# Optimization experiments

Hardware: AMD Instinct MI355X
Metric: run time of the kernel (lower is better)

## Reference

```python
import jax, jax.numpy as jnp
import numpy as np

D = 256; NHEAD = 8; NQ = 300; NLAYERS = 6; NLEV = 3; NPTS = 4
DFF = 1024; NCLS = 80; BS = 16
SPATIAL = ((80, 80), (40, 40), (20, 20))
LM = sum(h * w for h, w in SPATIAL)
DH = D // NHEAD
PARAM_NAMES = ['sa_wq','sa_bq','sa_wk','sa_bk','sa_wv','sa_bv','sa_wo','sa_bo',
               'ln1_g','ln1_b','ln2_g','ln2_b','ln3_g','ln3_b',
               'off_w','off_b','attw_w','attw_b','val_w','val_b','out_w','out_b',
               'ffn_w1','ffn_b1','ffn_w2','ffn_b2',
               'bb_w1','bb_b1','bb_w2','bb_b2','bb_w3','bb_b3',
               'sc_w','sc_b','qp_w1','qp_b1','qp_w2','qp_b2']


def _ln(x, g, b, eps=1e-5):
    m = x.mean(-1, keepdims=True)
    v = ((x - m) ** 2).mean(-1, keepdims=True)
    return (x - m) * jax.lax.rsqrt(v + eps) * g + b


def _mlp2(x, w1, b1, w2, b2):
    # 2-layer MLP, ReLU on hidden only (act_final_layer=False)
    return jnp.maximum(x @ w1 + b1, 0.0) @ w2 + b2


def _inv_sigmoid(x, eps=1e-5):
    x = jnp.clip(x, 0.0, 1.0)
    return jnp.log(jnp.clip(x, eps, None) / jnp.clip(1.0 - x, eps, None))


def _mha(q, k, v, wq, bq, wk, bk, wv, bv, wo, bo):
    B, N, _ = q.shape
    Q = (q @ wq + bq).reshape(B, N, NHEAD, DH)
    K = (k @ wk + bk).reshape(B, N, NHEAD, DH)
    V = (v @ wv + bv).reshape(B, N, NHEAD, DH)
    att = jnp.einsum('bqhd,bkhd->bhqk', Q, K) * (1.0 / np.sqrt(DH))
    att = jax.nn.softmax(att, axis=-1)
    o = jnp.einsum('bhqk,bkhd->bqhd', att, V).reshape(B, N, D)
    return o @ wo + bo


def _bilinear(v, x, y, Hl, Wl):
    # v: [B, Hl*Wl, C]; x, y: [B, M] pixel coords (align_corners=False, zero padding)
    x0 = jnp.floor(x); y0 = jnp.floor(y)
    wx = x - x0; wy = y - y0
    out = 0.0
    for dx, dy, w in ((0, 0, (1 - wx) * (1 - wy)), (1, 0, wx * (1 - wy)),
                      (0, 1, (1 - wx) * wy), (1, 1, wx * wy)):
        xi = x0 + dx; yi = y0 + dy
        valid = (xi >= 0) & (xi < Wl) & (yi >= 0) & (yi < Hl)
        lin = (jnp.clip(yi, 0, Hl - 1) * Wl + jnp.clip(xi, 0, Wl - 1)).astype(jnp.int32)
        g = jnp.take_along_axis(v, lin[..., None], axis=1)
        out = out + g * (w * valid)[..., None]
    return out


def _deform_attn(q, ref, memory, ow, ob, aw, ab, vw, vb, pw, pb):
    # q: [B,NQ,D]; ref: [B,NQ,4] cxcywh in [0,1]; memory: [B,LM,D]
    B = q.shape[0]
    value = (memory @ vw + vb).reshape(B, LM, NHEAD, DH)
    off = (q @ ow + ob).reshape(B, NQ, NHEAD, NLEV, NPTS, 2)
    attw = jax.nn.softmax((q @ aw + ab).reshape(B, NQ, NHEAD, NLEV * NPTS), -1)
    attw = attw.reshape(B, NQ, NHEAD, NLEV, NPTS)
    r = ref[:, :, None, None, None, :]
    loc = r[..., :2] + off / NPTS * r[..., 2:] * 0.5  # [B,NQ,H,LV,P,2]
    start = 0
    acc = 0.0
    for lv, (Hl, Wl) in enumerate(SPATIAL):
        v = value[:, start:start + Hl * Wl]  # [B, Hl*Wl, H, DH]
        v = v.transpose(0, 2, 1, 3).reshape(B * NHEAD, Hl * Wl, DH)
        g = loc[:, :, :, lv]  # [B,NQ,H,P,2]
        x = (g[..., 0] * Wl - 0.5).transpose(0, 2, 1, 3).reshape(B * NHEAD, NQ * NPTS)
        y = (g[..., 1] * Hl - 0.5).transpose(0, 2, 1, 3).reshape(B * NHEAD, NQ * NPTS)
        s = _bilinear(v, x, y, Hl, Wl).reshape(B, NHEAD, NQ, NPTS, DH)
        w = attw[:, :, :, lv].transpose(0, 2, 1, 3)  # [B,H,NQ,P]
        acc = acc + (s * w[..., None]).sum(3)  # [B,H,NQ,DH]
        start += Hl * Wl
    o = acc.transpose(0, 2, 1, 3).reshape(B, NQ, D)
    return o @ pw + pb


def _decoder(tgt, ref_points_unact, memory, p):
    ref_d = jax.nn.sigmoid(ref_points_unact)
    out = tgt
    for i in range(NLAYERS):
        pos = _mlp2(ref_d, p['qp_w1'], p['qp_b1'], p['qp_w2'], p['qp_b2'])
        q = out + pos
        t2 = _mha(q, q, out, p['sa_wq'][i], p['sa_bq'][i], p['sa_wk'][i], p['sa_bk'][i],
                  p['sa_wv'][i], p['sa_bv'][i], p['sa_wo'][i], p['sa_bo'][i])
        out = _ln(out + t2, p['ln1_g'][i], p['ln1_b'][i])
        t2 = _deform_attn(out + pos, ref_d, memory, p['off_w'][i], p['off_b'][i],
                          p['attw_w'][i], p['attw_b'][i], p['val_w'][i], p['val_b'][i],
                          p['out_w'][i], p['out_b'][i])
        out = _ln(out + t2, p['ln2_g'][i], p['ln2_b'][i])
        out = _ln(out + _mlp2(out, p['ffn_w1'][i], p['ffn_b1'][i], p['ffn_w2'][i], p['ffn_b2'][i]),
                  p['ln3_g'][i], p['ln3_b'][i])
        h = jnp.maximum(out @ p['bb_w1'][i] + p['bb_b1'][i], 0.0)
        h = jnp.maximum(h @ p['bb_w2'][i] + p['bb_b2'][i], 0.0)
        delta = h @ p['bb_w3'][i] + p['bb_b3'][i]
        ref_d = jax.nn.sigmoid(delta + _inv_sigmoid(ref_d))
    logits = out @ p['sc_w'][NLAYERS - 1] + p['sc_b'][NLAYERS - 1]
    return ref_d, logits


def setup_inputs():
    key = jax.random.key(0)
    keys = iter(jax.random.split(key, 64))
    def rn(shape, s=0.02):
        return jax.random.normal(next(keys), shape, jnp.float32) * s
    L = NLAYERS
    inp = {
        'tgt': rn((BS, NQ, D), 1.0),
        'ref_points_unact': rn((BS, NQ, 4), 1.0),
        'memory': rn((BS, LM, D), 1.0),
    }
    for n in ['sa_wq', 'sa_wk', 'sa_wv', 'sa_wo', 'val_w', 'out_w', 'bb_w1', 'bb_w2']:
        inp[n] = rn((L, D, D))
    for n in ['sa_bq', 'sa_bk', 'sa_bv', 'sa_bo', 'ln1_b', 'ln2_b', 'ln3_b',
              'val_b', 'out_b', 'ffn_b2', 'bb_b1', 'bb_b2']:
        inp[n] = jnp.zeros((L, D), jnp.float32)
    for n in ['ln1_g', 'ln2_g', 'ln3_g']:
        inp[n] = jnp.ones((L, D), jnp.float32)
    OFF = NHEAD * NLEV * NPTS * 2
    ATT = NHEAD * NLEV * NPTS
    inp['off_w'] = rn((L, D, OFF)); inp['off_b'] = rn((L, OFF), 0.1)
    inp['attw_w'] = rn((L, D, ATT)); inp['attw_b'] = jnp.zeros((L, ATT), jnp.float32)
    inp['ffn_w1'] = rn((L, D, DFF)); inp['ffn_b1'] = jnp.zeros((L, DFF), jnp.float32)
    inp['ffn_w2'] = rn((L, DFF, D))
    inp['bb_w3'] = rn((L, D, 4)); inp['bb_b3'] = jnp.zeros((L, 4), jnp.float32)
    inp['sc_w'] = rn((L, D, NCLS)); inp['sc_b'] = jnp.zeros((L, NCLS), jnp.float32)
    inp['qp_w1'] = rn((4, 2 * D)); inp['qp_b1'] = jnp.zeros((2 * D,), jnp.float32)
    inp['qp_w2'] = rn((2 * D, D)); inp['qp_b2'] = jnp.zeros((D,), jnp.float32)
    return inp


def reference(tgt, ref_points_unact, memory, sa_wq, sa_bq, sa_wk, sa_bk, sa_wv, sa_bv,
              sa_wo, sa_bo, ln1_g, ln1_b, ln2_g, ln2_b, ln3_g, ln3_b, off_w, off_b,
              attw_w, attw_b, val_w, val_b, out_w, out_b, ffn_w1, ffn_b1, ffn_w2, ffn_b2,
              bb_w1, bb_b1, bb_w2, bb_b2, bb_w3, bb_b3, sc_w, sc_b,
              qp_w1, qp_b1, qp_w2, qp_b2):
    _a = dict(locals())
    p = {k: _a[k] for k in PARAM_NAMES}
    ref_d, logits = _decoder(tgt, ref_points_unact, memory, p)
    # eval path: stacked final-layer outputs, shape [1, BS, NQ, 4] and [1, BS, NQ, NCLS]
    return ref_d[None], logits[None]
```

## Files before the change

### kernel.cpp

```cpp
#include <hip/hip_runtime.h>
#include <hip/hip_bf16.h>

typedef __hip_bfloat16 bf16;
typedef short short8 __attribute__((ext_vector_type(8)));
typedef short short4v __attribute__((ext_vector_type(4)));
typedef float float4v __attribute__((ext_vector_type(4)));

#define D_ 256
#define NHEAD_ 8
#define DH_ 32
#define NQ_ 300
#define NLAYERS_ 6
#define DFF_ 1024
#define NCLS_ 80
#define BS_ 16
#define LM_ 8400
#define BN_ (BS_*NQ_)

static __device__ __forceinline__ short f2bf(float x){
    union{float f; unsigned u;} v; v.f = x;
    unsigned r = v.u + 0x7FFF + ((v.u>>16)&1);
    return (short)(r>>16);
}
static __device__ __forceinline__ float bf2f(short s){
    union{unsigned u; float f;} v; v.u = ((unsigned)(unsigned short)s)<<16; return v.f;
}

#define LSTR 40

template<int TM, bool ABF16, bool RELU, bool OUTBF16>
__global__ __launch_bounds__(256) void mfma_gemm_kernel(
    const void* __restrict__ Av, const void* __restrict__ A2v,
    const void* __restrict__ A3v, int nA2lim,
    const short* __restrict__ WT, size_t zWT,
    const float* __restrict__ b0, const float* __restrict__ b1,
    const float* __restrict__ b2, int ns1, int ns2, size_t zB,
    void* __restrict__ Cv, size_t zC, int M, int K, int N, int nxt)
{
    __shared__ short As[2][TM*LSTR];
    __shared__ short Bs[2][128*LSTR];
    int zz, n0;
    if(nxt){ zz = blockIdx.x / nxt; n0 = (blockIdx.x % nxt)*128; }
    else   { zz = blockIdx.z;       n0 = blockIdx.x*128; }
    WT += (size_t)zz*zWT; b0 += (size_t)zz*zB; b1 += (size_t)zz*zB; b2 += (size_t)zz*zB;
    int tid = threadIdx.x;
    int lane = tid&63, wave = tid>>6;
    int m0 = blockIdx.y*TM;
    const int MI = TM/32;
    int wm = (wave>>1)*(TM/2), wn = (wave&1)*64;
    int lr = lane&15, lq = lane>>4;
    float4v acc[MI][4];
    #pragma unroll
    for(int i=0;i<MI;i++)
        #pragma unroll
        for(int j=0;j<4;j++){ acc[i][j].x=0.f; acc[i][j].y=0.f; acc[i][j].z=0.f; acc[i][j].w=0.f; }

    const float* Af; const float* Ad; const short* Ah;
    if(ABF16){ Ah = (const short*)Av; Af=nullptr; Ad=nullptr; }
    else {
        Af = (n0 < nA2lim)? (const float*)Av : (const float*)A3v;
        Ad = (n0 < nA2lim)? (const float*)A2v : nullptr;
        Ah = nullptr;
    }

    short8  rA16[ABF16? TM/64 : 1];
    float4v rAf [ABF16? 1 : TM/32];
    float4v rAd [ABF16? 1 : TM/32];
    short8  rB[2];

    auto LOAD = [&](int k0){
        if constexpr(ABF16){
            #pragma unroll
            for(int it=0; it<TM/64; ++it){
                int idx=(it*256+tid)*8; int r=idx>>5, kk=idx&31; int gm=m0+r;
                short8 v = {};
                if(gm<M) v = *(const short8*)(Ah + (size_t)gm*K + (k0+kk));
                rA16[it]=v;
            }
        } else {
            #pragma unroll
            for(int it=0; it<TM/32; ++it){
                int idx=(it*256+tid)*4; int r=idx>>5, kk=idx&31; int gm=m0+r;
                float4v v; v.x=0.f;v.y=0.f;v.z=0.f;v.w=0.f;
                float4v w; w.x=0.f;w.y=0.f;w.z=0.f;w.w=0.f;
                if(gm<M){
                    v = *(const float4v*)(Af + (size_t)gm*K + (k0+kk));
                    if(Ad) w = *(const float4v*)(Ad + (size_t)gm*K + (k0+kk));
                }
                rAf[it]=v; rAd[it]=w;
            }
        }
        #pragma unroll
        for(int it=0; it<2; ++it){
            int idx=(it*256+tid)*8; int r=idx>>5, kk=idx&31; int gn=n0+r;
            short8 v = {};
            if(gn<N) v = *(const short8*)(WT + (size_t)gn*K + (k0+kk));
            rB[it]=v;
        }
    };
    auto STORE = [&](int buf){
        if constexpr(ABF16){
            #pragma unroll
            for(int it=0; it<TM/64; ++it){
                int idx=(it*256+tid)*8; int r=idx>>5, kk=idx&31;
                *(short8*)(&As[buf][r*LSTR+kk]) = rA16[it];
            }
        } else {
            #pragma unroll
            for(int it=0; it<TM/32; ++it){
                int idx=(it*256+tid)*4; int r=idx>>5, kk=idx&31;
                float4v v = rAf[it];
                if(Ad){ v.x+=rAd[it].x; v.y+=rAd[it].y; v.z+=rAd[it].z; v.w+=rAd[it].w; }
                short4v h; h.x=f2bf(v.x); h.y=f2bf(v.y); h.z=f2bf(v.z); h.w=f2bf(v.w);
                *(short4v*)(&As[buf][r*LSTR+kk]) = h;
            }
        }
        #pragma unroll
        for(int it=0; it<2; ++it){
            int idx=(it*256+tid)*8; int r=idx>>5, kk=idx&31;
            *(short8*)(&Bs[buf][r*LSTR+kk]) = rB[it];
        }
    };

    const int nt = K>>5;
    LOAD(0);
    STORE(0);
    __syncthreads();
    for(int t=0; t<nt; ++t){
        int cb = t&1;
        if(t+1<nt) LOAD((t+1)<<5);
        short8 af[MI], bfr[4];
        #pragma unroll
        for(int mi=0;mi<MI;mi++) af[mi]  = *(const short8*)(&As[cb][(wm+mi*16+lr)*LSTR + lq*8]);
        #pragma unroll
        for(int ni=0;ni<4;ni++) bfr[ni] = *(const short8*)(&Bs[cb][(wn+ni*16+lr)*LSTR + lq*8]);
        #pragma unroll
        for(int mi=0;mi<MI;mi++)
            #pragma unroll
            for(int ni=0;ni<4;ni++)
                acc[mi][ni] = __builtin_amdgcn_mfma_f32_16x16x32_bf16(af[mi], bfr[ni], acc[mi][ni], 0,0,0);
        if(t+1<nt){
            STORE(cb^1);
            __syncthreads();
        }
    }
    float* Cf=(float*)Cv + (size_t)zz*zC; bf16* Ch=(bf16*)Cv + (size_t)zz*zC;
    #pragma unroll
    for(int mi=0;mi<MI;mi++){
        #pragma unroll
        for(int r=0;r<4;r++){
            int gm = m0+wm+mi*16+lq*4+r;
            if(gm>=M) continue;
            #pragma unroll
            for(int ni=0;ni<4;ni++){
                int gn = n0+wn+ni*16+lr;
                if(gn>=N) continue;
                float bv = (gn<ns1)? b0[gn] : ((gn<ns2)? b1[gn-ns1] : b2[gn-ns2]);
                float v = acc[mi][ni][r] + bv;
                if(RELU) v = fmaxf(v,0.f);
                if(OUTBF16) Ch[(size_t)gm*N+gn]=__float2bfloat16(v);
                else        Cf[(size_t)gm*N+gn]=v;
            }
        }
    }
}

__global__ __launch_bounds__(256) void fused_mha_kernel(
    const float* __restrict__ QKV, short* __restrict__ O)
{
    const int ld = 768;
    int bh = blockIdx.y; int b = bh>>3, h = bh&7;
    int q0 = blockIdx.x*64;
    __shared__ short lds[31104];
    short* Vts = lds;
    short* Qs  = lds + 10368;
    short* Ks  = lds + 12672;
    short* Ps  = lds + 10368;
    int tid = threadIdx.x;
    for(int idx=tid; idx<64*8; idx+=256){
        int r=idx>>3, c4=(idx&7)*4; int gq=q0+r;
        float4v v; v.x=0.f;v.y=0.f;v.z=0.f;v.w=0.f;
        if(gq<NQ_) v = *(const float4v*)(QKV + ((size_t)(b*NQ_+gq))*ld + h*DH_ + c4);
        short4v h4; h4.x=f2bf(v.x);h4.y=f2bf(v.y);h4.z=f2bf(v.z);h4.w=f2bf(v.w);
        *(short4v*)(Qs + r*36 + c4) = h4;
    }
    for(int idx=tid; idx<304*8; idx+=256){
        int r=idx>>3, c4=(idx&7)*4;
        float4v v; v.x=0.f;v.y=0.f;v.z=0.f;v.w=0.f;
        if(r<NQ_) v = *(const float4v*)(QKV + 256 + ((size_t)(b*NQ_+r))*ld + h*DH_ + c4);
        short4v h4; h4.x=f2bf(v.x);h4.y=f2bf(v.y);h4.z=f2bf(v.z);h4.w=f2bf(v.w);
        *(short4v*)(Ks + r*36 + c4) = h4;
    }
    for(int idx=tid; idx<320*8; idx+=256){
        int r=idx>>3, c4=(idx&7)*4;
        float4v v; v.x=0.f;v.y=0.f;v.z=0.f;v.w=0.f;
        if(r<NQ_) v = *(const float4v*)(QKV + 512 + ((size_t)(b*NQ_+r))*ld + h*DH_ + c4);
        Vts[(c4+0)*324+r]=f2bf(v.x); Vts[(c4+1)*324+r]=f2bf(v.y);
        Vts[(c4+2)*324+r]=f2bf(v.z); Vts[(c4+3)*324+r]=f2bf(v.w);
    }
    __syncthreads();

    int lane = tid&63, wave = tid>>6;
    int lr = lane&15, lq = lane>>4;
    int mrow = wave*16;
    const float scale = 0.17677669529663687f;

    float4v acc[19];
    #pragma unroll
    for(int t=0;t<19;t++){ acc[t].x=0.f; acc[t].y=0.f; acc[t].z=0.f; acc[t].w=0.f; }
    short8 afrag = *(const short8*)(&Qs[(mrow+lr)*36 + lq*8]);
    #pragma unroll
    for(int t=0;t<19;t++){
        short8 bfrag = *(const short8*)(&Ks[(t*16+lr)*36 + lq*8]);
        acc[t] = __builtin_amdgcn_mfma_f32_16x16x32_bf16(afrag, bfrag, acc[t], 0,0,0);
    }
    __syncthreads();

    for(int idx=tid; idx<64*16; idx+=256){
        int r=idx>>4, c=idx&15;
        Ps[r*324 + 304 + c]=0;
    }
    #pragma unroll
    for(int t=0;t<19;t++){
        #pragma unroll
        for(int r=0;r<4;r++) acc[t][r] *= scale;
    }
    if(lr>=12){
        #pragma unroll
        for(int r=0;r<4;r++) acc[18][r] = -1e30f;
    }
    float mx[4];
    #pragma unroll
    for(int r=0;r<4;r++){
        float m = acc[0][r];
        #pragma unroll
        for(int t=1;t<19;t++) m = fmaxf(m, acc[t][r]);
        m = fmaxf(m, __shfl_xor(m,1)); m = fmaxf(m, __shfl_xor(m,2));
        m = fmaxf(m, __shfl_xor(m,4)); m = fmaxf(m, __shfl_xor(m,8));
        mx[r]=m;
    }
    float sum[4] = {0.f,0.f,0.f,0.f};
    #pragma unroll
    for(int t=0;t<19;t++){
        #pragma unroll
        for(int r=0;r<4;r++){
            float p = __expf(acc[t][r]-mx[r]);
            acc[t][r]=p; sum[r]+=p;
        }
    }
    #pragma unroll
    for(int r=0;r<4;r++){
        float s = sum[r];
        s += __shfl_xor(s,1); s += __shfl_xor(s,2);
        s += __shfl_xor(s,4); s += __shfl_xor(s,8);
        sum[r] = 1.f/s;
    }
    #pragma unroll
    for(int t=0;t<19;t++){
        #pragma unroll
        for(int r=0;r<4;r++){
            Ps[(mrow + lq*4 + r)*324 + t*16 + lr] = f2bf(acc[t][r]*sum[r]);
        }
    }
    __syncthreads();
    float4v oacc[2];
    oacc[0].x=0.f;oacc[0].y=0.f;oacc[0].z=0.f;oacc[0].w=0.f;
    oacc[1]=oacc[0];
    #pragma unroll
    for(int kc=0;kc<10;kc++){
        short8 pa = *(const short8*)(&Ps[(mrow+lr)*324 + kc*32 + lq*8]);
        #pragma unroll
        for(int n=0;n<2;n++){
            short8 vb = *(const short8*)(&Vts[(n*16+lr)*324 + kc*32 + lq*8]);
            oacc[n] = __builtin_amdgcn_mfma_f32_16x16x32_bf16(pa, vb, oacc[n], 0,0,0);
        }
    }
    #pragma unroll
    for(int n=0;n<2;n++){
        #pragma unroll
        for(int r=0;r<4;r++){
            int gq = q0 + mrow + lq*4 + r;
            if(gq<NQ_)
                O[((size_t)(b*NQ_+gq))*D_ + h*DH_ + n*16 + lr] = f2bf(oacc[n][r]);
        }
    }
}

#define NTD 74
struct TD { const float* src; unsigned dstoff; int K, N, base; };
struct TAll { TD d[NTD]; };

__global__ __launch_bounds__(256) void transpose_all_kernel(TAll p, short* __restrict__ WTb){
    int blk = blockIdx.x;
    int di = 0;
    #pragma unroll 1
    for(int i=0;i<NTD;i++){ if(blk >= p.d[i].base) di = i; }
    TD d = p.d[di];
    int rel = blk - d.base;
    int ntx = (d.N+31)/32;
    int tn = (rel % ntx)*32, tk = (rel / ntx)*32;
    __shared__ float t[32][33];
    int tx = threadIdx.x&31, ty = threadIdx.x>>5;
    for(int i=0;i<32;i+=8){
        int k = tk+ty+i, n = tn+tx;
        t[ty+i][tx] = (k<d.K && n<d.N)? d.src[(size_t)k*d.N+n] : 0.f;
    }
    __syncthreads();
    short* out = WTb + d.dstoff;
    for(int i=0;i<32;i+=8){
        int n = tn+ty+i, k = tk+tx;
        if(n<d.N && k<d.K) out[(size_t)n*d.K+k] = f2bf(t[tx][ty+i]);
    }
}

template<bool RELU, bool BBOX>
__global__ __launch_bounds__(256) void gemm_kernel(
    const float* __restrict__ A, const float* __restrict__ W,
    const float* __restrict__ bias, float* __restrict__ Cf,
    int M, int K, int N)
{
    __shared__ float As[16][68];
    __shared__ float Bs[16][68];
    int tid = threadIdx.x;
    int m0 = blockIdx.y*64, n0 = blockIdx.x*64;
    int tm = tid>>4, tn = tid&15;
    float acc[4][4] = {};
    int lam = tid>>2;
    int lak = (tid&3)*4;
    int lbk = tid>>4;
    int lbn = (tid&15)*4;
    for(int k0=0;k0<K;k0+=16){
        {
            int m = m0+lam;
            #pragma unroll
            for(int j=0;j<4;j++){
                int k = k0+lak+j;
                float v=0.f;
                if(m<M && k<K) v = A[(size_t)m*K+k];
                As[lak+j][lam]=v;
            }
        }
        {
            int k = k0+lbk;
            #pragma unroll
            for(int j=0;j<4;j++){
                int n = n0+lbn+j;
                float v=0.f;
                if(k<K && n<N) v = W[(size_t)k*N+n];
                Bs[lbk][lbn+j]=v;
            }
        }
        __syncthreads();
        #pragma unroll
        for(int kk=0;kk<16;kk++){
            float a[4], bb[4];
            #pragma unroll
            for(int i=0;i<4;i++) a[i]=As[kk][tm*4+i];
            #pragma unroll
            for(int j=0;j<4;j++) bb[j]=Bs[kk][tn*4+j];
            #pragma unroll
            for(int i=0;i<4;i++)
                #pragma unroll
                for(int j=0;j<4;j++) acc[i][j] += a[i]*bb[j];
        }
        __syncthreads();
    }
    #pragma unroll
    for(int i=0;i<4;i++){
        int m=m0+tm*4+i; if(m>=M) continue;
        #pragma unroll
        for(int j=0;j<4;j++){
            int n=n0+tn*4+j; if(n>=N) continue;
            float v = acc[i][j] + bias[n];
            if(BBOX){
                float x = Cf[(size_t)m*N+n];
                x = fminf(fmaxf(x,0.f),1.f);
                float num = fmaxf(x,1e-5f), den = fmaxf(1.f-x,1e-5f);
                float nd = v + logf(num/den);
                Cf[(size_t)m*N+n] = 1.f/(1.f+expf(-nd));
            } else {
                if(RELU) v = fmaxf(v,0.f);
                Cf[(size_t)m*N+n]=v;
            }
        }
    }
}

__global__ void copy_kernel(const float* __restrict__ a, float* __restrict__ o, int n){
    int i = blockIdx.x*blockDim.x+threadIdx.x;
    if(i<n) o[i]=a[i];
}
__global__ void cvt_f32_bf16_kernel(const float* __restrict__ a, short* __restrict__ o, int n4){
    int i = blockIdx.x*blockDim.x+threadIdx.x;
    if(i<n4){
        float4v v = *(const float4v*)(a + (size_t)i*4);
        short4v h; h.x=f2bf(v.x); h.y=f2bf(v.y); h.z=f2bf(v.z); h.w=f2bf(v.w);
        *(short4v*)(o + (size_t)i*4) = h;
    }
}
__global__ void sigmoid_init_kernel(const float* __restrict__ a, float* __restrict__ o, int n){
    int i = blockIdx.x*blockDim.x+threadIdx.x;
    if(i<n){ float x=a[i]; o[i]=1.f/(1.f+expf(-x)); }
}
__global__ void write_out_kernel(const float* __restrict__ refd, const float* __restrict__ logits, float* __restrict__ out){
    int i = blockIdx.x*blockDim.x+threadIdx.x;
    if(i<BN_*4) out[i]=refd[i];
    else if(i<BN_*4+BN_*NCLS_) out[i]=logits[i-BN_*4];
}

__global__ __launch_bounds__(256) void ln_residual_kernel(
    float* __restrict__ cur, const short* __restrict__ t2b,
    const float* __restrict__ g, const float* __restrict__ b,
    short* __restrict__ cb)
{
    int row = blockIdx.x; int c = threadIdx.x;
    size_t idx = (size_t)row*D_+c;
    float x = cur[idx] + bf2f(t2b[idx]);
    float v1 = x, v2 = x*x;
    #pragma unroll
    for(int o=32;o>0;o>>=1){ v1 += __shfl_down(v1,o,64); v2 += __shfl_down(v2,o,64); }
    __shared__ float s1[4], s2[4], st[2];
    int wid=c>>6, lane=c&63;
    if(lane==0){ s1[wid]=v1; s2[wid]=v2; }
    __syncthreads();
    if(c==0){
        float a=0,d=0;
        #pragma unroll
        for(int i=0;i<4;i++){a+=s1[i]; d+=s2[i];}
        st[0]=a/(float)D_; st[1]=d/(float)D_;
    }
    __syncthreads();
    float m=st[0], var=st[1]-m*m;
    float y = (x-m)*rsqrtf(var+1e-5f)*g[c] + b[c];
    cur[idx]=y;
    if(cb) cb[idx]=f2bf(y);
}

__global__ __launch_bounds__(256) void deform_sample_kernel(
    const float* __restrict__ refd, const float* __restrict__ oab,
    const bf16* __restrict__ value, short* __restrict__ outacc)
{
    int row = blockIdx.x; int b = row/NQ_;
    int tid = threadIdx.x; int h = tid>>5, c = tid&31;
    __shared__ float so[192], sa[96], sr[4];
    if(tid<192) so[tid]=oab[(size_t)row*288+tid];
    if(tid<96)  sa[tid]=oab[(size_t)row*288+192+tid];
    if(tid<4)   sr[tid]=refd[(size_t)row*4+tid];
    __syncthreads();
    if(tid<8){
        float* p = sa + tid*12;
        float m=-1e30f;
        #pragma unroll
        for(int i2=0;i2<12;i2++) m=fmaxf(m,p[i2]);
        float s=0.f;
        #pragma unroll
        for(int i2=0;i2<12;i2++){ float e=__expf(p[i2]-m); p[i2]=e; s+=e; }
        float inv=1.f/s;
        #pragma unroll
        for(int i2=0;i2<12;i2++) p[i2]*=inv;
    }
    __syncthreads();
    float cx=sr[0], cy=sr[1], rw=sr[2], rh=sr[3];
    const int HS[3]={80,40,20}, WS[3]={80,40,20}, ST[3]={0,6400,8000};
    float acc=0.f;
    const bf16* vb = value + (size_t)b*LM_*D_ + h*DH_ + c;
    for(int lv=0;lv<3;lv++){
        int Hl=HS[lv], Wl=WS[lv], st=ST[lv];
        #pragma unroll
        for(int pt=0;pt<4;pt++){
            int oi = ((h*3+lv)*4+pt)*2;
            float ox=so[oi], oy=so[oi+1];
            float wa=sa[h*12+lv*4+pt];
            float lx = cx + ox*0.25f*rw*0.5f;
            float ly = cy + oy*0.25f*rh*0.5f;
            float x = lx*(float)Wl - 0.5f, y = ly*(float)Hl - 0.5f;
            float x0f=floorf(x), y0f=floorf(y);
            float wx=x-x0f, wy=y-y0f;
            int x0=(int)x0f, y0=(int)y0f;
            #pragma unroll
            for(int dy=0;dy<2;dy++){
                #pragma unroll
                for(int dx=0;dx<2;dx++){
                    int xi=x0+dx, yi=y0+dy;
                    if(xi>=0 && xi<Wl && yi>=0 && yi<Hl){
                        float w = (dx? wx : 1.f-wx)*(dy? wy : 1.f-wy);
                        int lin = yi*Wl+xi;
                        acc += __bfloat162float(vb[(size_t)(st+lin)*D_]) * (w*wa);
                    }
                }
            }
        }
    }
    outacc[(size_t)row*D_+tid]=f2bf(acc);
}

static void gemm_simt(const float*A, const float*W, const float*b, float*C,
                      int M,int K,int N, hipStream_t s, bool relu){
    dim3 g((N+63)/64,(M+63)/64);
    if(relu) gemm_kernel<true,false><<<g,256,0,s>>>(A,W,b,C,M,K,N);
    else     gemm_kernel<false,false><<<g,256,0,s>>>(A,W,b,C,M,K,N);
}
static void gemm_bbox(const float*A, const float*W, const float*b, float*refd,
                      int M,int K,int N, hipStream_t s){
    dim3 g((N+63)/64,(M+63)/64);
    gemm_kernel<false,true><<<g,256,0,s>>>(A,W,b,refd,M,K,N);
}
static void g64x(const void*A, const void*A2, const void*A3, int nA2lim,
                 const short*WT, const float*b0, const float*b1, const float*b2,
                 int ns1, int ns2, void*C, int M,int K,int N,
                 bool abf16, bool relu, bool outbf, hipStream_t s){
    dim3 g((N+127)/128,(M+63)/64,1);
    #define CALLG(AB,RL,OB) mfma_gemm_kernel<64,AB,RL,OB><<<g,256,0,s>>>(A,A2,A3,nA2lim,WT,0,b0,b1,b2,ns1,ns2,0,C,0,M,K,N,0)
    if(abf16){
        if(relu){ if(outbf) CALLG(true,true,true);  else CALLG(true,true,false); }
        else    { if(outbf) CALLG(true,false,true); else CALLG(true,false,false); }
    } else {
        if(relu){ if(outbf) CALLG(false,true,true);  else CALLG(false,true,false); }
        else    { if(outbf) CALLG(false,false,true); else CALLG(false,false,false); }
    }
    #undef CALLG
}
static void g64(const float*A, const float*A2, const float*A3, int nA2lim,
                const short*WT, const float*b0, const float*b1, const float*b2,
                int ns1, int ns2, void*C, int M,int K,int N,
                bool relu, bool outbf, hipStream_t s){
    g64x(A,A2,A3,nA2lim,WT,b0,b1,b2,ns1,ns2,C,M,K,N,false,relu,outbf,s);
}
static void g64b(const short*A, const short*WT, const float*b, void*C,
                 int M,int K,int N, hipStream_t s){
    g64x(A,nullptr,nullptr,1<<30,WT,b,b,b,N,N+1,C,M,K,N,true,false,true,s);
}
static int ntiles(int K,int N){ return ((N+31)/32)*((K+31)/32); }

extern "C" void kernel_launch(void* const* d_in, const int* in_sizes, int n_in,
                              void* d_out, int out_size, void* d_ws, size_t ws_size,
                              hipStream_t stream) {
    const float* tgt   = (const float*)d_in[0];
    const float* rpu   = (const float*)d_in[1];
    const float* mem   = (const float*)d_in[2];
    const float* sa_wq = (const float*)d_in[3];
    const float* sa_wk = (const float*)d_in[4];
    const float* sa_wv = (const float*)d_in[5];
    const float* sa_wo = (const float*)d_in[6];
    const float* val_w = (const float*)d_in[7];
    const float* out_w = (const float*)d_in[8];
    const float* bb_w1 = (const float*)d_in[9];
    const float* bb_w2 = (const float*)d_in[10];
    const float* sa_bq = (const float*)d_in[11];
    const float* sa_bk = (const float*)d_in[12];
    const float* sa_bv = (const float*)d_in[13];
    const float* sa_bo = (const float*)d_in[14];
    const float* ln1_b = (const float*)d_in[15];
    const float* ln2_b = (const float*)d_in[16];
    const float* ln3_b = (const float*)d_in[17];
    const float* val_b = (const float*)d_in[18];
    const float* out_b = (const float*)d_in[19];
    const float* ffn_b2= (const float*)d_in[20];
    const float* bb_b1 = (const float*)d_in[21];
    const float* bb_b2 = (const float*)d_in[22];
    const float* ln1_g = (const float*)d_in[23];
    const float* ln2_g = (const float*)d_in[24];
    const float* ln3_g = (const float*)d_in[25];
    const float* off_w = (const float*)d_in[26];
    const float* off_b = (const float*)d_in[27];
    const float* attw_w= (const float*)d_in[28];
    const float* attw_b= (const float*)d_in[29];
    const float* ffn_w1= (const float*)d_in[30];
    const float* ffn_b1= (const float*)d_in[31];
    const float* ffn_w2= (const float*)d_in[32];
    const float* bb_w3 = (const float*)d_in[33];
    const float* bb_b3 = (const float*)d_in[34];
    const float* sc_w  = (const float*)d_in[35];
    const float* sc_b  = (const float*)d_in[36];
    const float* qp_w1 = (const float*)d_in[37];
    const float* qp_b1 = (const float*)d_in[38];
    const float* qp_w2 = (const float*)d_in[39];
    const float* qp_b2 = (const float*)d_in[40];

    const size_t BND = (size_t)BN_*D_;
    const size_t USZ = (size_t)BN_*DFF_;
    const size_t LMD = (size_t)BS_*LM_*D_;
    const size_t LSZ = 1122304;

    float* ws   = (float*)d_ws;
    float* cur  = ws;
    float* pos  = cur + BND;
    float* refd = pos + BND;
    float* U    = refd + (size_t)BN_*4;
    short* tmp16 = (short*)(U + USZ);
    short* t216  = tmp16 + BND;
    short* WT    = t216 + BND;
    short* qp2T  = WT + 6*LSZ;
    short* scT   = qp2T + 131072;
    short* X     = scT + 20480;
    float* hid512 = U;
    float* QKVh   = U;
    float* offsb  = U;
    short* ffnh16 = (short*)U;
    short* bb1b   = (short*)U;
    float* bb2    = U + BND;
    float* logitsb= U;
    short* curb = tmp16;

    size_t offX = (size_t)((char*)X - (char*)d_ws);
    int vmode;
    if(ws_size >= offX + 7*LMD*2)      vmode = 3;
    else if(ws_size >= offX + 6*LMD*2) vmode = 2;
    else if(ws_size >= offX + 4*LMD)   vmode = 1;
    else                               vmode = 0;
    short* memT   = X;
    short* values = (vmode==3)? X + LMD : X;
    short* value1 = X + LMD;
    short* value0 = X;

    const int nBN_D = (int)BND;
    copy_kernel<<<(nBN_D+255)/256,256,0,stream>>>(tgt, cur, nBN_D);
    sigmoid_init_kernel<<<(BN_*4+255)/256,256,0,stream>>>(rpu, refd, BN_*4);
    if(vmode==1 || vmode==3){
        int n4 = (int)(LMD/4);
        cvt_f32_bf16_kernel<<<(n4+255)/256,256,0,stream>>>(mem, memT, n4);
    }

    {
        TAll tp; int base=0; int di=0;
        const size_t offs[12] = { 0,65536,131072,196608,262144,327680,
                                  393216,442368,466944,729088,991232,1056768 };
        const int Ks[12] = { 256,256,256,256,256,256,256,256,256,1024,256,256 };
        const int Ns[12] = { 256,256,256,256,256,256,192,96,1024,256,256,256 };
        for(int l=0;l<NLAYERS_;l++){
            const float* srcs[12] = { sa_wq+(size_t)l*D_*D_, sa_wk+(size_t)l*D_*D_, sa_wv+(size_t)l*D_*D_,
                                      sa_wo+(size_t)l*D_*D_, val_w+(size_t)l*D_*D_, out_w+(size_t)l*D_*D_,
                                      off_w+(size_t)l*D_*192, attw_w+(size_t)l*D_*96,
                                      ffn_w1+(size_t)l*D_*DFF_, ffn_w2+(size_t)l*DFF_*D_,
                                      bb_w1+(size_t)l*D_*D_, bb_w2+(size_t)l*D_*D_ };
            for(int j=0;j<12;j++){
                tp.d[di] = { srcs[j], (unsigned)(l*LSZ + offs[j]), Ks[j], Ns[j], base };
                base += ntiles(Ks[j],Ns[j]); di++;
            }
        }
        tp.d[di] = { qp_w2, (unsigned)(6*LSZ), 512, 256, base }; base += ntiles(512,256); di++;
        tp.d[di] = { sc_w + (size_t)(NLAYERS_-1)*D_*NCLS_, (unsigned)(6*LSZ+131072), 256, 80, base }; base += ntiles(256,80); di++;
        transpose_all_kernel<<<base,256,0,stream>>>(tp, WT);
    }

    if(vmode==3){
        dim3 g(12,1050,1);
        mfma_gemm_kernel<128,true,false,true><<<g,256,0,stream>>>(
            memT,nullptr,nullptr,1<<30, WT+262144, LSZ,
            val_b,val_b,val_b, 256,257, 256, values, LMD, BS_*LM_, D_, D_, 2);
    } else if(vmode==2){
        dim3 g(12,1050,1);
        mfma_gemm_kernel<128,false,false,true><<<g,256,0,stream>>>(
            mem,nullptr,mem,1<<30, WT+262144, LSZ,
            val_b,val_b,val_b, 256,257, 256, values, LMD, BS_*LM_, D_, D_, 2);
    }

    for(int i=0;i<NLAYERS_;i++){
        const bf16* value_i;
        if(vmode>=2) value_i = (const bf16*)(values + (size_t)i*LMD);
        else {
            dim3 g(2,1050,1);
            if(vmode==1){
                mfma_gemm_kernel<128,true,false,true><<<g,256,0,stream>>>(
                    memT,nullptr,nullptr,1<<30, WT+i*LSZ+262144, 0,
                    val_b+(size_t)i*D_,val_b,val_b, 256,257, 0, value1, 0, BS_*LM_, D_, D_, 0);
                value_i = (const bf16*)value1;
            } else {
                mfma_gemm_kernel<128,false,false,true><<<g,256,0,stream>>>(
                    mem,nullptr,mem,1<<30, WT+i*LSZ+262144, 0,
                    val_b+(size_t)i*D_,val_b,val_b, 256,257, 0, value0, 0, BS_*LM_, D_, D_, 0);
                value_i = (const bf16*)value0;
            }
        }
        gemm_simt(refd, qp_w1, qp_b1, hid512, BN_, 4, 512, stream, true);
        g64(hid512,nullptr,hid512,1<<30, qp2T, qp_b2,qp_b2,qp_b2, 256,257,
            pos, BN_, 512, D_, false,false, stream);
        g64(cur, pos, cur, 512, WT+i*LSZ,
            sa_bq+(size_t)i*D_, sa_bk+(size_t)i*D_, sa_bv+(size_t)i*D_, 256, 512,
            QKVh, BN_, D_, 768, false,false, stream);
        {
            dim3 g((NQ_+63)/64, BS_*NHEAD_);
            fused_mha_kernel<<<g,256,0,stream>>>(QKVh, tmp16);
        }
        g64b(tmp16, WT+i*LSZ+196608, sa_bo+(size_t)i*D_, t216, BN_, D_, D_, stream);
        ln_residual_kernel<<<BN_,256,0,stream>>>(cur, t216, ln1_g+(size_t)i*D_, ln1_b+(size_t)i*D_, nullptr);
        g64(cur, pos, cur, 1<<30, WT+i*LSZ+393216,
            off_b+(size_t)i*192, attw_b+(size_t)i*96, attw_b+(size_t)i*96, 192, 288,
            offsb, BN_, D_, 288, false,false, stream);
        deform_sample_kernel<<<BN_,256,0,stream>>>(refd, offsb, value_i, tmp16);
        g64b(tmp16, WT+i*LSZ+327680, out_b+(size_t)i*D_, t216, BN_, D_, D_, stream);
        ln_residual_kernel<<<BN_,256,0,stream>>>(cur, t216, ln2_g+(size_t)i*D_, ln2_b+(size_t)i*D_, curb);
        g64x(curb,nullptr,nullptr,1<<30, WT+i*LSZ+466944, ffn_b1+(size_t)i*DFF_,ffn_b1,ffn_b1, DFF_,DFF_+1,
             ffnh16, BN_, D_, DFF_, true,true,true, stream);
        g64x(ffnh16,nullptr,nullptr,1<<30, WT+i*LSZ+729088, ffn_b2+(size_t)i*D_,ffn_b2,ffn_b2, 256,257,
             t216, BN_, DFF_, D_, true,false,true, stream);
        ln_residual_kernel<<<BN_,256,0,stream>>>(cur, t216, ln3_g+(size_t)i*D_, ln3_b+(size_t)i*D_, curb);
        g64x(curb,nullptr,nullptr,1<<30, WT+i*LSZ+991232, bb_b1+(size_t)i*D_,bb_b1,bb_b1, 256,257,
             bb1b, BN_, D_, D_, true,true,true, stream);
        g64x(bb1b,nullptr,nullptr,1<<30, WT+i*LSZ+1056768, bb_b2+(size_t)i*D_,bb_b2,bb_b2, 256,257,
             bb2, BN_, D_, D_, true,true,false, stream);
        gemm_bbox(bb2, bb_w3+(size_t)i*D_*4, bb_b3+(size_t)i*4, refd, BN_, D_, 4, stream);
    }
    g64x(curb,nullptr,nullptr,1<<30, scT, sc_b+(size_t)(NLAYERS_-1)*NCLS_,sc_b,sc_b, NCLS_,NCLS_+1,
         logitsb, BN_, D_, NCLS_, true,false,false, stream);
    int tot = BN_*4 + BN_*NCLS_;
    write_out_kernel<<<(tot+255)/256,256,0,stream>>>(refd, logitsb, (float*)d_out);
}
```

Measured before the change: 2.586 ms.

## Add 64x64 full-K-chunk MFMA GEMM with XCD-aware block remapping

Adds a new bf16 MFMA GEMM kernel that uses 64x64 output tiles and loads 128-wide K chunks into LDS, so there are fewer barriers per tile. It remaps a 1-D grid so consecutive tiles land on the same XCD, which should improve L2 reuse of shared A rows and weights. All per-layer projections and the batched value projection (vmode 3) now go through this kernel instead of the 64x128 tiled one. In exchange it drops the double buffering of the old kernel and uses smaller N tiles, which can mean more total blocks and less load/compute overlap.

```diff
diff --git a/kernel.cpp b/kernel.cpp
--- a/kernel.cpp
+++ b/kernel.cpp
@@ -24,6 +24,120 @@
 }
 static __device__ __forceinline__ float bf2f(short s){
     union{unsigned u; float f;} v; v.u = ((unsigned)(unsigned short)s)<<16; return v.f;
+}
+
+#define KC_ 128
+#define LK_ 136
+
+template<bool ABF16, bool RELU, bool OUTBF16>
+__global__ __launch_bounds__(256) void fullk_gemm_kernel(
+    const void* __restrict__ Av, const void* __restrict__ A2v,
+    const void* __restrict__ A3v, int nA2lim,
+    const short* __restrict__ WT, size_t zWT,
+    const float* __restrict__ b0, const float* __restrict__ b1,
+    const float* __restrict__ b2, int ns1, int ns2, size_t zB,
+    void* __restrict__ Cv, size_t zC, int M, int K, int N, int nn, int nz)
+{
+    __shared__ short As[64*LK_];
+    __shared__ short Bs[64*LK_];
+    int nwg = gridDim.x;
+    int orig = blockIdx.x;
+    int q = nwg>>3, rr = nwg&7, xcd = orig&7, jj = orig>>3;
+    int bid = (xcd<rr ? xcd*(q+1) : rr*(q+1)+(xcd-rr)*q) + jj;
+    int per = nn*nz;
+    int mt  = bid/per; int rem = bid - mt*per;
+    int zz  = rem/nn;  int n0  = (rem - zz*nn)*64;
+    int m0  = mt*64;
+    WT += (size_t)zz*zWT; b0 += (size_t)zz*zB; b1 += (size_t)zz*zB; b2 += (size_t)zz*zB;
+    int tid = threadIdx.x;
+    int lane = tid&63, wave = tid>>6;
+    int wm = (wave>>1)*32, wn = (wave&1)*32;
+    int lr = lane&15, lq = lane>>4;
+    float4v acc[2][2];
+    #pragma unroll
+    for(int i=0;i<2;i++)
+        #pragma unroll
+        for(int j=0;j<2;j++){ acc[i][j].x=0.f; acc[i][j].y=0.f; acc[i][j].z=0.f; acc[i][j].w=0.f; }
+
+    const float* Af=nullptr; const float* Ad=nullptr; const short* Ah=nullptr;
+    if(ABF16){ Ah = (const short*)Av; }
+    else {
+        Af = (n0 < nA2lim)? (const float*)Av : (const float*)A3v;
+        Ad = (n0 < nA2lim)? (const float*)A2v : nullptr;
+    }
+
+    for(int kc=0; kc<K; kc+=KC_){
+        if(kc) __syncthreads();
+        if(ABF16){
+            #pragma unroll
+            for(int it=0; it<4; ++it){
+                int c = it*256+tid;
+                int r = c>>4, k8 = (c&15)*8;
+                int gm = m0+r;
+                short8 v = {};
+                if(gm<M) v = *(const short8*)(Ah + (size_t)gm*K + kc + k8);
+                *(short8*)(&As[r*LK_ + k8]) = v;
+            }
+        } else {
+            #pragma unroll
+            for(int it=0; it<8; ++it){
+                int c = it*256+tid;
+                int r = c>>5, k4 = (c&31)*4;
+                int gm = m0+r;
+                float4v v; v.x=0.f;v.y=0.f;v.z=0.f;v.w=0.f;
+                if(gm<M){
+                    v = *(const float4v*)(Af + (size_t)gm*K + kc + k4);
+                    if(Ad){
+                        float4v w = *(const float4v*)(Ad + (size_t)gm*K + kc + k4);
+                        v.x+=w.x; v.y+=w.y; v.z+=w.z; v.w+=w.w;
+                    }
+                }
+                short4v h; h.x=f2bf(v.x); h.y=f2bf(v.y); h.z=f2bf(v.z); h.w=f2bf(v.w);
+                *(short4v*)(&As[r*LK_ + k4]) = h;
+            }
+        }
+        #pragma unroll
+        for(int it=0; it<4; ++it){
+            int c = it*256+tid;
+            int r = c>>4, k8 = (c&15)*8;
+            int gn = n0+r;
+            short8 v = {};
+            if(gn<N) v = *(const short8*)(WT + (size_t)gn*K + kc + k8);
+            *(short8*)(&Bs[r*LK_ + k8]) = v;
+        }
+        __syncthreads();
+        #pragma unroll
+        for(int t=0;t<KC_/32;t++){
+            int ko = t*32 + lq*8;
+            short8 af0 = *(const short8*)(&As[(wm+lr)*LK_ + ko]);
+            short8 af1 = *(const short8*)(&As[(wm+16+lr)*LK_ + ko]);
+            short8 bf0 = *(const short8*)(&Bs[(wn+lr)*LK_ + ko]);
+            short8 bf1 = *(const short8*)(&Bs[(wn+16+lr)*LK_ + ko]);
+            acc[0][0] = __builtin_amdgcn_mfma_f32_16x16x32_bf16(af0, bf0, acc[0][0], 0,0,0);
+            acc[0][1] = __builtin_amdgcn_mfma_f32_16x16x32_bf16(af0, bf1, acc[0][1], 0,0,0);
+            acc[1][0] = __builtin_amdgcn_mfma_f32_16x16x32_bf16(af1, bf0, acc[1][0], 0,0,0);
+            acc[1][1] = __builtin_amdgcn_mfma_f32_16x16x32_bf16(af1, bf1, acc[1][1], 0,0,0);
+        }
+    }
+    float* Cf=(float*)Cv + (size_t)zz*zC; bf16* Ch=(bf16*)Cv + (size_t)zz*zC;
+    #pragma unroll
+    for(int mi=0;mi<2;mi++){
+        #pragma unroll
+        for(int r=0;r<4;r++){
+            int gm = m0+wm+mi*16+lq*4+r;
+            if(gm>=M) continue;
+            #pragma unroll
+            for(int ni=0;ni<2;ni++){
+                int gn = n0+wn+ni*16+lr;
+                if(gn>=N) continue;
+                float bv = (gn<ns1)? b0[gn] : ((gn<ns2)? b1[gn-ns1] : b2[gn-ns2]);
+                float v = acc[mi][ni][r] + bv;
+                if(RELU) v = fmaxf(v,0.f);
+                if(OUTBF16) Ch[(size_t)gm*N+gn]=__float2bfloat16(v);
+                else        Cf[(size_t)gm*N+gn]=v;
+            }
+        }
+    }
 }
 
 #define LSTR 40
@@ -505,30 +619,21 @@
     dim3 g((N+63)/64,(M+63)/64);
     gemm_kernel<false,true><<<g,256,0,s>>>(A,W,b,refd,M,K,N);
 }
-static void g64x(const void*A, const void*A2, const void*A3, int nA2lim,
-                 const short*WT, const float*b0, const float*b1, const float*b2,
-                 int ns1, int ns2, void*C, int M,int K,int N,
-                 bool abf16, bool relu, bool outbf, hipStream_t s){
-    dim3 g((N+127)/128,(M+63)/64,1);
-    #define CALLG(AB,RL,OB) mfma_gemm_kernel<64,AB,RL,OB><<<g,256,0,s>>>(A,A2,A3,nA2lim,WT,0,b0,b1,b2,ns1,ns2,0,C,0,M,K,N,0)
-    if(abf16){
-        if(relu){ if(outbf) CALLG(true,true,true);  else CALLG(true,true,false); }
-        else    { if(outbf) CALLG(true,false,true); else CALLG(true,false,false); }
-    } else {
-        if(relu){ if(outbf) CALLG(false,true,true);  else CALLG(false,true,false); }
-        else    { if(outbf) CALLG(false,false,true); else CALLG(false,false,false); }
-    }
-    #undef CALLG
-}
-static void g64(const float*A, const float*A2, const float*A3, int nA2lim,
+static void gfk(const void*A, const void*A2, const void*A3, int nA2lim,
                 const short*WT, const float*b0, const float*b1, const float*b2,
                 int ns1, int ns2, void*C, int M,int K,int N,
-                bool relu, bool outbf, hipStream_t s){
-    g64x(A,A2,A3,nA2lim,WT,b0,b1,b2,ns1,ns2,C,M,K,N,false,relu,outbf,s);
-}
-static void g64b(const short*A, const short*WT, const float*b, void*C,
-                 int M,int K,int N, hipStream_t s){
-    g64x(A,nullptr,nullptr,1<<30,WT,b,b,b,N,N+1,C,M,K,N,true,false,true,s);
+                bool abf16, bool relu, bool outbf, hipStream_t s){
+    int nn=(N+63)/64, nm=(M+63)/64;
+    dim3 g(nm*nn);
+    #define CF(AB,RL,OB) fullk_gemm_kernel<AB,RL,OB><<<g,256,0,s>>>(A,A2,A3,nA2lim,WT,0,b0,b1,b2,ns1,ns2,0,C,0,M,K,N,nn,1)
+    if(abf16){
+        if(relu){ if(outbf) CF(true,true,true);  else CF(true,true,false); }
+        else    { if(outbf) CF(true,false,true); else CF(true,false,false); }
+    } else {
+        if(relu){ if(outbf) CF(false,true,true);  else CF(false,true,false); }
+        else    { if(outbf) CF(false,false,true); else CF(false,false,false); }
+    }
+    #undef CF
 }
 static int ntiles(int K,int N){ return ((N+31)/32)*((K+31)/32); }
 
@@ -644,10 +749,10 @@
     }
 
     if(vmode==3){
-        dim3 g(12,1050,1);
-        mfma_gemm_kernel<128,true,false,true><<<g,256,0,stream>>>(
+        dim3 g((BS_*LM_/64)*4*6);
+        fullk_gemm_kernel<true,false,true><<<g,256,0,stream>>>(
             memT,nullptr,nullptr,1<<30, WT+262144, LSZ,
-            val_b,val_b,val_b, 256,257, 256, values, LMD, BS_*LM_, D_, D_, 2);
+            val_b,val_b,val_b, 256,257, 256, values, LMD, BS_*LM_, D_, D_, 4, 6);
     } else if(vmode==2){
         dim3 g(12,1050,1);
         mfma_gemm_kernel<128,false,false,true><<<g,256,0,stream>>>(
@@ -673,36 +778,40 @@
             }
         }
         gemm_simt(refd, qp_w1, qp_b1, hid512, BN_, 4, 512, stream, true);
-        g64(hid512,nullptr,hid512,1<<30, qp2T, qp_b2,qp_b2,qp_b2, 256,257,
-            pos, BN_, 512, D_, false,false, stream);
-        g64(cur, pos, cur, 512, WT+i*LSZ,
+        gfk(hid512,nullptr,hid512,1<<30, qp2T, qp_b2,qp_b2,qp_b2, 256,257,
+            pos, BN_, 512, D_, false,false,false, stream);
+        gfk(cur, pos, cur, 512, WT+i*LSZ,
             sa_bq+(size_t)i*D_, sa_bk+(size_t)i*D_, sa_bv+(size_t)i*D_, 256, 512,
-            QKVh, BN_, D_, 768, false,false, stream);
+            QKVh, BN_, D_, 768, false,false,false, stream);
         {
             dim3 g((NQ_+63)/64, BS_*NHEAD_);
             fused_mha_kernel<<<g,256,0,stream>>>(QKVh, tmp16);
         }
-        g64b(tmp16, WT+i*LSZ+196608, sa_bo+(size_t)i*D_, t216, BN_, D_, D_, stream);
+        gfk(tmp16,nullptr,nullptr,1<<30, WT+i*LSZ+196608,
+            sa_bo+(size_t)i*D_,sa_bo,sa_bo, 256,257, t216, BN_, D_, D_,
+            true,false,true, stream);
         ln_residual_kernel<<<BN_,256,0,stream>>>(cur, t216, ln1_g+(size_t)i*D_, ln1_b+(size_t)i*D_, nullptr);
-        g64(cur, pos, cur, 1<<30, WT+i*LSZ+393216,
+        gfk(cur, pos, cur, 1<<30, WT+i*LSZ+393216,
             off_b+(size_t)i*192, attw_b+(size_t)i*96, attw_b+(size_t)i*96, 192, 288,
-            offsb, BN_, D_, 288, false,false, stream);
+            offsb, BN_, D_, 288, false,false,false, stream);
         deform_sample_kernel<<<BN_,256,0,stream>>>(refd, offsb, value_i, tmp16);
-        g64b(tmp16, WT+i*LSZ+327680, out_b+(size_t)i*D_, t216, BN_, D_, D_, stream);
+        gfk(tmp16,nullptr,nullptr,1<<30, WT+i*LSZ+327680,
+            out_b+(size_t)i*D_,out_b,out_b, 256,257, t216, BN_, D_, D_,
+            true,false,true, stream);
         ln_residual_kernel<<<BN_,256,0,stream>>>(cur, t216, ln2_g+(size_t)i*D_, ln2_b+(size_t)i*D_, curb);
-        g64x(curb,nullptr,nullptr,1<<30, WT+i*LSZ+466944, ffn_b1+(size_t)i*DFF_,ffn_b1,ffn_b1, DFF_,DFF_+1,
-             ffnh16, BN_, D_, DFF_, true,true,true, stream);
-        g64x(ffnh16,nullptr,nullptr,1<<30, WT+i*LSZ+729088, ffn_b2+(size_t)i*D_,ffn_b2,ffn_b2, 256,257,
-             t216, BN_, DFF_, D_, true,false,true, stream);
+        gfk(curb,nullptr,nullptr,1<<30, WT+i*LSZ+466944, ffn_b1+(size_t)i*DFF_,ffn_b1,ffn_b1, DFF_,DFF_+1,
+            ffnh16, BN_, D_, DFF_, true,true,true, stream);
+        gfk(ffnh16,nullptr,nullptr,1<<30, WT+i*LSZ+729088, ffn_b2+(size_t)i*D_,ffn_b2,ffn_b2, 256,257,
+            t216, BN_, DFF_, D_, true,false,true, stream);
         ln_residual_kernel<<<BN_,256,0,stream>>>(cur, t216, ln3_g+(size_t)i*D_, ln3_b+(size_t)i*D_, curb);
-        g64x(curb,nullptr,nullptr,1<<30, WT+i*LSZ+991232, bb_b1+(size_t)i*D_,bb_b1,bb_b1, 256,257,
-             bb1b, BN_, D_, D_, true,true,true, stream);
-        g64x(bb1b,nullptr,nullptr,1<<30, WT+i*LSZ+1056768, bb_b2+(size_t)i*D_,bb_b2,bb_b2, 256,257,
-             bb2, BN_, D_, D_, true,true,false, stream);
+        gfk(curb,nullptr,nullptr,1<<30, WT+i*LSZ+991232, bb_b1+(size_t)i*D_,bb_b1,bb_b1, 256,257,
+            bb1b, BN_, D_, D_, true,true,true, stream);
+        gfk(bb1b,nullptr,nullptr,1<<30, WT+i*LSZ+1056768, bb_b2+(size_t)i*D_,bb_b2,bb_b2, 256,257,
+            bb2, BN_, D_, D_, true,true,false, stream);
         gemm_bbox(bb2, bb_w3+(size_t)i*D_*4, bb_b3+(size_t)i*4, refd, BN_, D_, 4, stream);
     }
-    g64x(curb,nullptr,nullptr,1<<30, scT, sc_b+(size_t)(NLAYERS_-1)*NCLS_,sc_b,sc_b, NCLS_,NCLS_+1,
-         logitsb, BN_, D_, NCLS_, true,false,false, stream);
+    gfk(curb,nullptr,nullptr,1<<30, scT, sc_b+(size_t)(NLAYERS_-1)*NCLS_,sc_b,sc_b, NCLS_,NCLS_+1,
+        logitsb, BN_, D_, NCLS_, true,false,false, stream);
     int tot = BN_*4 + BN_*NCLS_;
     write_out_kernel<<<(tot+255)/256,256,0,stream>>>(refd, logitsb, (float*)d_out);
 }
```

After: 2.945 ms. +13.9%, slower.
